# Kernel tuning notes

Measured on AMD Instinct MI355X. Metric: run time of the kernel, lower is better.

The kernel has to match this reference:

```python
import jax, jax.numpy as jnp
import numpy as np

D = 1024  # input_size
NORM = 1.0 / np.sqrt(D)


def setup_inputs() -> dict:
    key = jax.random.key(0)
    k_x, k_q, k_k, k_v = jax.random.split(key, 4)
    B, S = 4, 2048
    scale = 1.0 / np.sqrt(D)  # init ~ nn.Linear default magnitude
    return {
        "inputs": jax.random.normal(k_x, (B, S, D), dtype=jnp.float32),
        "Wq": jax.random.uniform(k_q, (D, D), jnp.float32, -scale, scale),
        "Wk": jax.random.uniform(k_k, (D, D), jnp.float32, -scale, scale),
        "Wv": jax.random.uniform(k_v, (D, D), jnp.float32, -scale, scale),
    }


def reference(inputs, Wq, Wk, Wv):
    # nn.Linear(x) = x @ W.T (no bias)
    Q = jnp.einsum("bsd,ed->bse", inputs, Wq)
    K = jnp.einsum("bsd,ed->bse", inputs, Wk)
    V = jnp.einsum("bsd,ed->bse", inputs, Wv)
    attn = jnp.einsum("bqe,bke->bqk", Q, K) * NORM  # [B,S,S]
    attn = jax.nn.softmax(attn, axis=2)
    return jnp.einsum("bqk,bke->bqe", attn, V)
```

## Files before the change

kernel.cpp:

```cpp
#include <hip/hip_runtime.h>

typedef __bf16 bf16_t;
typedef __bf16 bf16x8 __attribute__((ext_vector_type(8)));
typedef __bf16 bf16x4 __attribute__((ext_vector_type(4)));
typedef float  floatx4 __attribute__((ext_vector_type(4)));

#define BM 128
#define BN 128
#define BK 64

__device__ __forceinline__ void gload_lds16(const bf16_t* g, bf16_t* l) {
    __builtin_amdgcn_global_load_lds(
        (const __attribute__((address_space(1))) void*)g,
        (__attribute__((address_space(3))) void*)l,
        16, 0, 0);
}

template <int MODE, typename OutT>
__global__ __launch_bounds__(256) void gemm_nt(
    const bf16_t* __restrict__ A, int lda, size_t batchA,
    const bf16_t* __restrict__ B, int ldb, size_t batchB,
    OutT* __restrict__ C, int ldc, size_t batchC,
    bf16_t* __restrict__ C2, int ldc2,
    const float* __restrict__ rowinv, int batchR,
    int K, float scale)
{
    __shared__ bf16_t sA[BM * BK];
    __shared__ bf16_t sB[BN * BK];

    A += (size_t)blockIdx.z * batchA;
    B += (size_t)blockIdx.z * batchB;

    const int tid  = threadIdx.x;
    const int wid  = tid >> 6;
    const int lane = tid & 63;

    const int bm = blockIdx.x * BM;
    const int bn = blockIdx.y * BN;

    const int rr  = tid >> 3;
    const int kc8 = (((tid & 7) ^ (rr & 7)) << 3);

    const int wy = (wid >> 1) * 64;
    const int wx = (wid & 1) * 64;
    const int lr = lane & 15;

    floatx4 acc[4][4] = {};

    const bf16_t* pa = A + (size_t)(bm + rr) * lda + kc8;
    const bf16_t* pb = B + (size_t)(bn + rr) * ldb + kc8;
    bf16_t* la = &sA[wid * 512];
    bf16_t* lb = &sB[wid * 512];

    for (int k0 = 0; k0 < K; k0 += BK) {
        #pragma unroll
        for (int c = 0; c < 4; ++c) {
            gload_lds16(pa + (size_t)(c * 32) * lda + k0, la + c * 2048);
            gload_lds16(pb + (size_t)(c * 32) * ldb + k0, lb + c * 2048);
        }
        __syncthreads();

        #pragma unroll
        for (int kk = 0; kk < 2; ++kk) {
            const int cch = (kk << 2) + (lane >> 4);
            bf16x8 af[4], bq[4];
            #pragma unroll
            for (int i = 0; i < 4; ++i) {
                int r = wy + i * 16 + lr;
                af[i] = *(const bf16x8*)&sA[(r << 6) + ((cch ^ (r & 7)) << 3)];
            }
            #pragma unroll
            for (int j = 0; j < 4; ++j) {
                int r = wx + j * 16 + lr;
                bq[j] = *(const bf16x8*)&sB[(r << 6) + ((cch ^ (r & 7)) << 3)];
            }
            #pragma unroll
            for (int i = 0; i < 4; ++i)
                #pragma unroll
                for (int j = 0; j < 4; ++j)
                    acc[i][j] = __builtin_amdgcn_mfma_f32_16x16x32_bf16(
                        bq[j], af[i], acc[i][j], 0, 0, 0);
        }
        __syncthreads();
    }

    const int cfix = lane & 15;
    const int creg = (lane >> 4) << 2;

    if constexpr (MODE == 1) {
        if (blockIdx.z == 2) {
            #pragma unroll
            for (int i = 0; i < 4; ++i) {
                int mg = bm + wy + i * 16 + cfix;
                #pragma unroll
                for (int j = 0; j < 4; ++j) {
                    int ng = bn + wx + j * 16 + creg;
                    #pragma unroll
                    for (int r = 0; r < 4; ++r)
                        C2[(size_t)(ng + r) * ldc2 + mg] = (bf16_t)acc[i][j][r];
                }
            }
            return;
        }
        OutT* Cz = C + (size_t)blockIdx.z * batchC;
        #pragma unroll
        for (int i = 0; i < 4; ++i) {
            size_t row = (size_t)(bm + wy + i * 16 + cfix);
            #pragma unroll
            for (int j = 0; j < 4; ++j) {
                int col = bn + wx + j * 16 + creg;
                bf16x4 v;
                #pragma unroll
                for (int r = 0; r < 4; ++r) v[r] = (bf16_t)acc[i][j][r];
                *(bf16x4*)&Cz[row * (size_t)ldc + col] = v;
            }
        }
    } else if constexpr (MODE == 2) {
        OutT* Cz = C + (size_t)blockIdx.z * batchC;
        #pragma unroll
        for (int i = 0; i < 4; ++i) {
            size_t row = (size_t)(bm + wy + i * 16 + cfix);
            #pragma unroll
            for (int j = 0; j < 4; ++j) {
                int col = bn + wx + j * 16 + creg;
                bf16x4 v;
                #pragma unroll
                for (int r = 0; r < 4; ++r)
                    v[r] = (bf16_t)__expf(acc[i][j][r] * scale);
                *(bf16x4*)&Cz[row * (size_t)ldc + col] = v;
            }
        }
    } else {
        OutT* Cz = C + (size_t)blockIdx.z * batchC;
        const float* rz = rowinv + (size_t)blockIdx.z * batchR;
        #pragma unroll
        for (int i = 0; i < 4; ++i) {
            int rloc = bm + wy + i * 16 + cfix;
            float rinv = rz[rloc];
            size_t row = (size_t)rloc;
            #pragma unroll
            for (int j = 0; j < 4; ++j) {
                int col = bn + wx + j * 16 + creg;
                floatx4 v;
                #pragma unroll
                for (int r = 0; r < 4; ++r) v[r] = acc[i][j][r] * rinv;
                *(floatx4*)&Cz[row * (size_t)ldc + col] = v;
            }
        }
    }
}

__global__ __launch_bounds__(256) void cvt_all(
    const float* __restrict__ X, const float* __restrict__ Wq,
    const float* __restrict__ Wk, const float* __restrict__ Wv,
    bf16_t* __restrict__ Xb, bf16_t* __restrict__ Wqb,
    bf16_t* __restrict__ Wkb, bf16_t* __restrict__ Wvb,
    int nX4, int nW4)
{
    int i = blockIdx.x * blockDim.x + threadIdx.x;
    const float* src; bf16_t* dst; int idx;
    if (i < nX4) { src = X; dst = Xb; idx = i; }
    else {
        int j = i - nX4;
        int w = j / nW4;
        idx = j - w * nW4;
        if (i >= nX4 + 3 * nW4) return;
        src = (w == 0) ? Wq : (w == 1) ? Wk : Wv;
        dst = (w == 0) ? Wqb : (w == 1) ? Wkb : Wvb;
    }
    float4 v = ((const float4*)src)[idx];
    bf16x4 o;
    o[0] = (bf16_t)v.x; o[1] = (bf16_t)v.y; o[2] = (bf16_t)v.z; o[3] = (bf16_t)v.w;
    *(bf16x4*)(dst + (size_t)idx * 4) = o;
}

__global__ __launch_bounds__(256) void rowsum_inv(
    const bf16_t* __restrict__ Sc, float* __restrict__ inv)
{
    const int row  = blockIdx.x * 4 + (threadIdx.x >> 6);
    const int lane = threadIdx.x & 63;
    const bf16_t* p = Sc + (size_t)row * 2048;
    float s = 0.f;
    #pragma unroll
    for (int c = 0; c < 4; ++c) {
        bf16x8 v = *(const bf16x8*)&p[c * 512 + lane * 8];
        #pragma unroll
        for (int r = 0; r < 8; ++r) s += (float)v[r];
    }
    #pragma unroll
    for (int off = 32; off >= 1; off >>= 1) s += __shfl_xor(s, off);
    if (lane == 0) inv[row] = 1.0f / s;
}

extern "C" void kernel_launch(void* const* d_in, const int* in_sizes, int n_in,
                              void* d_out, int out_size, void* d_ws, size_t ws_size,
                              hipStream_t stream)
{
    (void)in_sizes; (void)n_in; (void)out_size; (void)ws_size;
    const float* X  = (const float*)d_in[0];
    const float* Wq = (const float*)d_in[1];
    const float* Wk = (const float*)d_in[2];
    const float* Wv = (const float*)d_in[3];
    float* out = (float*)d_out;

    const int Bb = 4, S = 2048, D = 1024;
    const int M = Bb * S;

    char* ws = (char*)d_ws;
    size_t off = 0;
    auto carve = [&](size_t bytes) -> char* {
        char* p = ws + off;
        off += (bytes + 255) & ~(size_t)255;
        return p;
    };
    bf16_t* Xb  = (bf16_t*)carve((size_t)M * D * 2);
    bf16_t* Wqb = (bf16_t*)carve((size_t)D * D * 2);
    bf16_t* Wkb = (bf16_t*)carve((size_t)D * D * 2);
    bf16_t* Wvb = (bf16_t*)carve((size_t)D * D * 2);
    bf16_t* Qb  = (bf16_t*)carve((size_t)M * D * 2);
    bf16_t* Kb  = (bf16_t*)carve((size_t)M * D * 2);
    bf16_t* Vt  = (bf16_t*)carve((size_t)D * M * 2);
    bf16_t* Sc  = (bf16_t*)carve((size_t)Bb * S * S * 2);
    float*  inv = (float*)carve((size_t)M * 4);

    const int nX4 = M * D / 4, nW4 = D * D / 4;
    const int tot4 = nX4 + 3 * nW4;
    cvt_all<<<(tot4 + 255) / 256, 256, 0, stream>>>(
        X, Wq, Wk, Wv, Xb, Wqb, Wkb, Wvb, nX4, nW4);

    gemm_nt<1, bf16_t><<<dim3(M / BM, D / BN, 3), 256, 0, stream>>>(
        Xb, D, 0, Wqb, D, (size_t)D * D, Qb, D, (size_t)M * D,
        Vt, M, nullptr, 0, D, 1.0f);

    gemm_nt<2, bf16_t><<<dim3(S / BM, S / BN, Bb), 256, 0, stream>>>(
        Qb, D, (size_t)S * D, Kb, D, (size_t)S * D, Sc, S, (size_t)S * S,
        nullptr, 0, nullptr, 0, D, 0.03125f);

    rowsum_inv<<<Bb * S / 4, 256, 0, stream>>>(Sc, inv);

    gemm_nt<3, float><<<dim3(S / BM, D / BN, Bb), 256, 0, stream>>>(
        Sc, S, (size_t)S * S, Vt, M, (size_t)S, out, D, (size_t)S * D,
        nullptr, 0, inv, S, S, 1.0f);
}
```

Baseline: 244.7 us.

## Fuse softmax row-sum into score GEMM epilogue and widen K tile for PV GEMM

Accumulates exp row sums in the QK^T epilogue via warp shuffles and atomicAdd into a zeroed buffer, removing the separate row-sum kernel that re-read the full score matrix. The PV GEMM computes the reciprocal inline and is instantiated with a 128-wide K tile to halve loop iterations and barriers. Costs are atomic traffic, an extra memset, and doubled LDS per block for the PV GEMM which may lower occupancy.

```diff
diff --git a/kernel.cpp b/kernel.cpp
--- a/kernel.cpp
+++ b/kernel.cpp
@@ -4,10 +4,6 @@
 typedef __bf16 bf16x8 __attribute__((ext_vector_type(8)));
 typedef __bf16 bf16x4 __attribute__((ext_vector_type(4)));
 typedef float  floatx4 __attribute__((ext_vector_type(4)));
-
-#define BM 128
-#define BN 128
-#define BK 64
 
 __device__ __forceinline__ void gload_lds16(const bf16_t* g, bf16_t* l) {
     __builtin_amdgcn_global_load_lds(
@@ -16,17 +12,21 @@
         16, 0, 0);
 }
 
-template <int MODE, typename OutT>
+template <int MODE, int BKT, typename OutT>
 __global__ __launch_bounds__(256) void gemm_nt(
     const bf16_t* __restrict__ A, int lda, size_t batchA,
     const bf16_t* __restrict__ B, int ldb, size_t batchB,
     OutT* __restrict__ C, int ldc, size_t batchC,
     bf16_t* __restrict__ C2, int ldc2,
-    const float* __restrict__ rowinv, int batchR,
+    float* __restrict__ rowsums, int batchR,
     int K, float scale)
 {
-    __shared__ bf16_t sA[BM * BK];
-    __shared__ bf16_t sB[BN * BK];
+    constexpr int CH  = BKT / 8;
+    constexpr int RPS = 2048 / BKT;
+    constexpr int NSHOT = 128 / RPS;
+
+    __shared__ bf16_t sA[128 * BKT];
+    __shared__ bf16_t sB[128 * BKT];
 
     A += (size_t)blockIdx.z * batchA;
     B += (size_t)blockIdx.z * batchB;
@@ -35,11 +35,11 @@
     const int wid  = tid >> 6;
     const int lane = tid & 63;
 
-    const int bm = blockIdx.x * BM;
-    const int bn = blockIdx.y * BN;
-
-    const int rr  = tid >> 3;
-    const int kc8 = (((tid & 7) ^ (rr & 7)) << 3);
+    const int bm = blockIdx.x * 128;
+    const int bn = blockIdx.y * 128;
+
+    const int rr  = tid / CH;
+    const int kc8 = (((tid & (CH - 1)) ^ (rr & (CH - 1))) << 3);
 
     const int wy = (wid >> 1) * 64;
     const int wx = (wid & 1) * 64;
@@ -52,27 +52,27 @@
     bf16_t* la = &sA[wid * 512];
     bf16_t* lb = &sB[wid * 512];
 
-    for (int k0 = 0; k0 < K; k0 += BK) {
-        #pragma unroll
-        for (int c = 0; c < 4; ++c) {
-            gload_lds16(pa + (size_t)(c * 32) * lda + k0, la + c * 2048);
-            gload_lds16(pb + (size_t)(c * 32) * ldb + k0, lb + c * 2048);
+    for (int k0 = 0; k0 < K; k0 += BKT) {
+        #pragma unroll
+        for (int c = 0; c < NSHOT; ++c) {
+            gload_lds16(pa + (size_t)(c * RPS) * lda + k0, la + c * 2048);
+            gload_lds16(pb + (size_t)(c * RPS) * ldb + k0, lb + c * 2048);
         }
         __syncthreads();
 
         #pragma unroll
-        for (int kk = 0; kk < 2; ++kk) {
+        for (int kk = 0; kk < BKT / 32; ++kk) {
             const int cch = (kk << 2) + (lane >> 4);
             bf16x8 af[4], bq[4];
             #pragma unroll
             for (int i = 0; i < 4; ++i) {
                 int r = wy + i * 16 + lr;
-                af[i] = *(const bf16x8*)&sA[(r << 6) + ((cch ^ (r & 7)) << 3)];
+                af[i] = *(const bf16x8*)&sA[r * BKT + ((cch ^ (r & (CH - 1))) << 3)];
             }
             #pragma unroll
             for (int j = 0; j < 4; ++j) {
                 int r = wx + j * 16 + lr;
-                bq[j] = *(const bf16x8*)&sB[(r << 6) + ((cch ^ (r & 7)) << 3)];
+                bq[j] = *(const bf16x8*)&sB[r * BKT + ((cch ^ (r & (CH - 1))) << 3)];
             }
             #pragma unroll
             for (int i = 0; i < 4; ++i)
@@ -117,6 +117,8 @@
         }
     } else if constexpr (MODE == 2) {
         OutT* Cz = C + (size_t)blockIdx.z * batchC;
+        float* sums = rowsums + (size_t)blockIdx.z * batchR;
+        float rs[4] = {0.f, 0.f, 0.f, 0.f};
         #pragma unroll
         for (int i = 0; i < 4; ++i) {
             size_t row = (size_t)(bm + wy + i * 16 + cfix);
@@ -125,18 +127,30 @@
                 int col = bn + wx + j * 16 + creg;
                 bf16x4 v;
                 #pragma unroll
-                for (int r = 0; r < 4; ++r)
+                for (int r = 0; r < 4; ++r) {
                     v[r] = (bf16_t)__expf(acc[i][j][r] * scale);
+                    rs[i] += (float)v[r];
+                }
                 *(bf16x4*)&Cz[row * (size_t)ldc + col] = v;
             }
+        }
+        #pragma unroll
+        for (int i = 0; i < 4; ++i) {
+            rs[i] += __shfl_xor(rs[i], 16);
+            rs[i] += __shfl_xor(rs[i], 32);
+        }
+        if (lane < 16) {
+            #pragma unroll
+            for (int i = 0; i < 4; ++i)
+                atomicAdd(&sums[bm + wy + i * 16 + lane], rs[i]);
         }
     } else {
         OutT* Cz = C + (size_t)blockIdx.z * batchC;
-        const float* rz = rowinv + (size_t)blockIdx.z * batchR;
+        const float* sums = rowsums + (size_t)blockIdx.z * batchR;
         #pragma unroll
         for (int i = 0; i < 4; ++i) {
             int rloc = bm + wy + i * 16 + cfix;
-            float rinv = rz[rloc];
+            float rinv = 1.0f / sums[rloc];
             size_t row = (size_t)rloc;
             #pragma unroll
             for (int j = 0; j < 4; ++j) {
@@ -174,24 +188,6 @@
     *(bf16x4*)(dst + (size_t)idx * 4) = o;
 }
 
-__global__ __launch_bounds__(256) void rowsum_inv(
-    const bf16_t* __restrict__ Sc, float* __restrict__ inv)
-{
-    const int row  = blockIdx.x * 4 + (threadIdx.x >> 6);
-    const int lane = threadIdx.x & 63;
-    const bf16_t* p = Sc + (size_t)row * 2048;
-    float s = 0.f;
-    #pragma unroll
-    for (int c = 0; c < 4; ++c) {
-        bf16x8 v = *(const bf16x8*)&p[c * 512 + lane * 8];
-        #pragma unroll
-        for (int r = 0; r < 8; ++r) s += (float)v[r];
-    }
-    #pragma unroll
-    for (int off = 32; off >= 1; off >>= 1) s += __shfl_xor(s, off);
-    if (lane == 0) inv[row] = 1.0f / s;
-}
-
 extern "C" void kernel_launch(void* const* d_in, const int* in_sizes, int n_in,
                               void* d_out, int out_size, void* d_ws, size_t ws_size,
                               hipStream_t stream)
@@ -221,24 +217,24 @@
     bf16_t* Kb  = (bf16_t*)carve((size_t)M * D * 2);
     bf16_t* Vt  = (bf16_t*)carve((size_t)D * M * 2);
     bf16_t* Sc  = (bf16_t*)carve((size_t)Bb * S * S * 2);
-    float*  inv = (float*)carve((size_t)M * 4);
+    float*  sums = (float*)carve((size_t)M * 4);
+
+    hipMemsetAsync(sums, 0, (size_t)M * 4, stream);
 
     const int nX4 = M * D / 4, nW4 = D * D / 4;
     const int tot4 = nX4 + 3 * nW4;
     cvt_all<<<(tot4 + 255) / 256, 256, 0, stream>>>(
         X, Wq, Wk, Wv, Xb, Wqb, Wkb, Wvb, nX4, nW4);
 
-    gemm_nt<1, bf16_t><<<dim3(M / BM, D / BN, 3), 256, 0, stream>>>(
+    gemm_nt<1, 64, bf16_t><<<dim3(M / 128, D / 128, 3), 256, 0, stream>>>(
         Xb, D, 0, Wqb, D, (size_t)D * D, Qb, D, (size_t)M * D,
         Vt, M, nullptr, 0, D, 1.0f);
 
-    gemm_nt<2, bf16_t><<<dim3(S / BM, S / BN, Bb), 256, 0, stream>>>(
+    gemm_nt<2, 64, bf16_t><<<dim3(S / 128, S / 128, Bb), 256, 0, stream>>>(
         Qb, D, (size_t)S * D, Kb, D, (size_t)S * D, Sc, S, (size_t)S * S,
-        nullptr, 0, nullptr, 0, D, 0.03125f);
-
-    rowsum_inv<<<Bb * S / 4, 256, 0, stream>>>(Sc, inv);
-
-    gemm_nt<3, float><<<dim3(S / BM, D / BN, Bb), 256, 0, stream>>>(
+        nullptr, 0, sums, S, D, 0.03125f);
+
+    gemm_nt<3, 128, float><<<dim3(S / 128, D / 128, Bb), 256, 0, stream>>>(
         Sc, S, (size_t)S * S, Vt, M, (size_t)S, out, D, (size_t)S * D,
-        nullptr, 0, inv, S, S, 1.0f);
-}
+        nullptr, 0, sums, S, S, 1.0f);
+}
```

After: 242.9 us. Within noise of the previous version (-0.8%).
